# Kernel optimization log

Measured on AMD Instinct MI355X. Metric: run time of the kernel, lower is better.

The kernel has to match this reference:

```python
import jax, jax.numpy as jnp
import numpy as np

MARGIN = 0.3


def setup_inputs() -> dict:
    key = jax.random.key(0)
    k1, k2 = jax.random.split(key)
    inputs = jax.random.normal(k1, (8192, 256), dtype=jnp.float32)
    targets = jax.random.randint(k2, (8192,), 0, 512, dtype=jnp.int64)
    return {"inputs": inputs, "targets": targets}


def reference(inputs, targets):
    # L2-normalize features (normalize_feature=True default)
    x = inputs / (jnp.linalg.norm(inputs, axis=-1, keepdims=True) + 1e-12)
    n = x.shape[0]
    # pairwise euclidean distance [n, n]
    sq = jnp.sum(x * x, axis=1)
    dist = sq[:, None] + sq[None, :] - 2.0 * (x @ x.T)
    dist = jnp.sqrt(jnp.clip(dist, 1e-12, None))
    # positive / negative masks
    same = targets[:, None] == targets[None, :]
    eye = jnp.eye(n, dtype=bool)
    is_same = same & ~eye          # positives, diagonal excluded
    is_diff = ~same                # negatives
    neg_inf = jnp.float32(-jnp.inf)
    pos_inf = jnp.float32(jnp.inf)
    # hard positive: max over positives per row (fallback 0.0 if none)
    dist_ap = jnp.max(jnp.where(is_same, dist, neg_inf), axis=1)
    dist_ap = jnp.where(jnp.any(is_same, axis=1), dist_ap, 0.0)
    # hard negative: min over negatives per row (fallback margin+1 if none)
    dist_an = jnp.min(jnp.where(is_diff, dist, pos_inf), axis=1)
    dist_an = jnp.where(jnp.any(is_diff, axis=1), dist_an, MARGIN + 1.0)
    # MarginRankingLoss with y=1: mean(max(0, -(an - ap) + margin))
    loss = jnp.mean(jnp.maximum(0.0, dist_ap - dist_an + MARGIN))
    return loss
```

## Files before the change

### kernel.cpp

```cpp
#include <hip/hip_runtime.h>
#include <hip/hip_bf16.h>

#define NROWS  8192
#define DIM    256
#define MARGIN 0.3f

using bf16x8 = __attribute__((ext_vector_type(8))) short;
using f32x4  = __attribute__((ext_vector_type(4))) float;

__device__ inline ushort f2bf(float f) {
    __hip_bfloat16 h = __float2bfloat16(f);
    return *reinterpret_cast<ushort*>(&h);
}
__device__ inline float bf2f(ushort u) {
    return __uint_as_float(((unsigned)u) << 16);
}
__device__ inline unsigned f2ord(float f) {
    unsigned b = __float_as_uint(f);
    return (b & 0x80000000u) ? ~b : (b | 0x80000000u);
}
__device__ inline float ord2f(unsigned u) {
    return __uint_as_float((u & 0x80000000u) ? (u & 0x7FFFFFFFu) : ~u);
}
__device__ inline void ld16_g2l(const void* g, void* l) {
    __builtin_amdgcn_global_load_lds(
        (const __attribute__((address_space(1))) unsigned int*)g,
        (__attribute__((address_space(3))) unsigned int*)l, 16, 0, 0);
}

#define XBS_OFF 0u
#define SQS_OFF 4194304u
#define PMX_OFF 4259840u
#define NMN_OFF 4292608u
#define ACC_OFF 4327424u
#define TIK_OFF 4327432u

__global__ __launch_bounds__(256) void norm_kernel(
    const float* __restrict__ in, ushort* __restrict__ xbs,
    float* __restrict__ sqs, unsigned* __restrict__ pmax,
    unsigned* __restrict__ nmin, double* __restrict__ accd,
    unsigned* __restrict__ ticket)
{
    int row  = blockIdx.x * 4 + (threadIdx.x >> 6);
    int lane = threadIdx.x & 63;
    if (blockIdx.x == 0 && threadIdx.x == 0) { *accd = 0.0; *ticket = 0u; }
    float4 v = ((const float4*)(in + (size_t)row * DIM))[lane];
    float ss = v.x * v.x + v.y * v.y + v.z * v.z + v.w * v.w;
#pragma unroll
    for (int m = 1; m < 64; m <<= 1) ss += __shfl_xor(ss, m, 64);
    float inv = 1.0f / (sqrtf(ss) + 1e-12f);

    ushort4 st;
    st.x = f2bf(v.x * inv); st.y = f2bf(v.y * inv);
    st.z = f2bf(v.z * inv); st.w = f2bf(v.w * inv);

    ((ushort4*)(xbs + (size_t)row * DIM))[lane] = st;

    float a0 = bf2f(st.x), a1 = bf2f(st.y), a2 = bf2f(st.z), a3 = bf2f(st.w);
    float s2 = a0 * a0 + a1 * a1 + a2 * a2 + a3 * a3;
#pragma unroll
    for (int m = 1; m < 64; m <<= 1) s2 += __shfl_xor(s2, m, 64);
    if (lane == 0) {
        sqs[row]  = s2;
        pmax[row] = 0x007FFFFFu;
        nmin[row] = 0xFF800000u;
    }
}

__global__ __launch_bounds__(256, 2) void gram_kernel(
    const ushort* __restrict__ xbs, const float* __restrict__ sqs,
    const int* __restrict__ tgt, unsigned* __restrict__ pmax,
    unsigned* __restrict__ nmin)
{
    __shared__ struct {
        char  buf[2][16384];
        float sqc[512];
        int   tgc[512];
        int   tga[256];
    } sm;

    const int wave = threadIdx.x >> 6;
    const int lane = threadIdx.x & 63;
    const int l15  = lane & 15;
    const int quad = lane >> 4;
    const int mbase = blockIdx.x * 256 + wave * 64;
    const int nbase = blockIdx.y * 512;

    {
        int c = threadIdx.x * 2;
        sm.sqc[c]     = sqs[nbase + c];
        sm.sqc[c + 1] = sqs[nbase + c + 1];
        sm.tgc[c]     = tgt[nbase + c];
        sm.tgc[c + 1] = tgt[nbase + c + 1];
        sm.tga[threadIdx.x] = tgt[blockIdx.x * 256 + threadIdx.x];
    }

    bf16x8 afrag[4][8];
#pragma unroll
    for (int a = 0; a < 4; ++a) {
        const ushort* arow = xbs + (size_t)(mbase + a * 16 + l15) * DIM + quad * 8;
#pragma unroll
        for (int kk = 0; kk < 8; ++kk)
            afrag[a][kk] = *(const bf16x8*)(arow + kk * 32);
    }

    const int colh = lane >> 5, c31 = lane & 31;
    int offs[4];
#pragma unroll
    for (int j = 0; j < 4; ++j)
        offs[j] = colh * 512 + ((c31 ^ ((2 * j + colh) & 7)) << 4);

    const char* xbs_b = (const char*)xbs;

    {
        const char* gbase = xbs_b + (size_t)nbase * 512;
#pragma unroll
        for (int j = 0; j < 4; ++j) {
            int i = wave * 4 + j;
            ld16_g2l(gbase + i * 1024 + offs[j], sm.buf[0] + i * 1024);
        }
    }
    __syncthreads();

    float pm[16], nm[16];
#pragma unroll
    for (int j = 0; j < 16; ++j) { pm[j] = -__builtin_inff(); nm[j] = __builtin_inff(); }

#pragma unroll 2
    for (int s = 0; s < 16; ++s) {
        if (s < 15) {
            const char* gbase = xbs_b + (size_t)(nbase + (s + 1) * 32) * 512;
            char* lbase = sm.buf[(s + 1) & 1];
#pragma unroll
            for (int j = 0; j < 4; ++j) {
                int i = wave * 4 + j;
                ld16_g2l(gbase + i * 1024 + offs[j], lbase + i * 1024);
            }
        }
        const char* bufc = sm.buf[s & 1];
#pragma unroll
        for (int u = 0; u < 2; ++u) {
            const int t16 = s * 32 + u * 16;
            bf16x8 bfrag[8];
#pragma unroll
            for (int kk = 0; kk < 8; ++kk)
                bfrag[kk] = *(const bf16x8*)(bufc + u * 8192 + l15 * 512 +
                                             (((quad + 4 * kk) ^ (l15 & 7)) << 4));
            f32x4 acc4[4];
#pragma unroll
            for (int a = 0; a < 4; ++a) {
                f32x4 acc = {0.f, 0.f, 0.f, 0.f};
#pragma unroll
                for (int kk = 0; kk < 8; ++kk)
                    acc = __builtin_amdgcn_mfma_f32_16x16x32_bf16(afrag[a][kk], bfrag[kk], acc, 0, 0, 0);
                acc4[a] = acc;
            }
            const float sqc = sm.sqc[t16 + l15];
            const int   tc  = sm.tgc[t16 + l15];
#pragma unroll
            for (int a = 0; a < 4; ++a)
#pragma unroll
                for (int i = 0; i < 4; ++i) {
                    const float v = fmaf(acc4[a][i], -2.0f, sqc);
                    const bool same = (sm.tga[wave * 64 + a * 16 + quad * 4 + i] == tc);
                    pm[a * 4 + i] = fmaxf(pm[a * 4 + i], same ? v : -__builtin_inff());
                    nm[a * 4 + i] = fminf(nm[a * 4 + i], same ? __builtin_inff() : v);
                }
        }
        __syncthreads();
    }

#pragma unroll
    for (int m = 1; m < 16; m <<= 1) {
#pragma unroll
        for (int j = 0; j < 16; ++j) {
            pm[j] = fmaxf(pm[j], __shfl_xor(pm[j], m, 64));
            nm[j] = fminf(nm[j], __shfl_xor(nm[j], m, 64));
        }
    }
    if (l15 == 0) {
#pragma unroll
        for (int a = 0; a < 4; ++a)
#pragma unroll
            for (int i = 0; i < 4; ++i) {
                int r = mbase + a * 16 + quad * 4 + i;
                atomicMax(&pmax[r], f2ord(pm[a * 4 + i]));
                atomicMin(&nmin[r], f2ord(nm[a * 4 + i]));
            }
    }
}

__global__ __launch_bounds__(256) void finalize_kernel(
    const unsigned* __restrict__ pmax, const unsigned* __restrict__ nmin,
    const float* __restrict__ sqs, double* __restrict__ accd,
    unsigned* __restrict__ ticket, float* __restrict__ out)
{
    int r = blockIdx.x * 256 + threadIdx.x;
    float pe = ord2f(pmax[r]);
    float ne = ord2f(nmin[r]);
    float ap = sqrtf(fmaxf(sqs[r] + pe, 0.0f));
    float an = (ne > 1e30f) ? (MARGIN + 1.0f) : sqrtf(fmaxf(sqs[r] + ne, 0.0f));
    float h  = fmaxf(ap - an + MARGIN, 0.0f);
    double s = (double)h;
#pragma unroll
    for (int m = 1; m < 64; m <<= 1) s += __shfl_xor(s, m, 64);
    __shared__ double sh[4];
    if ((threadIdx.x & 63) == 0) sh[threadIdx.x >> 6] = s;
    __syncthreads();
    if (threadIdx.x == 0) {
        double b = sh[0] + sh[1] + sh[2] + sh[3];
        atomicAdd(accd, b);
        __threadfence();
        unsigned old = atomicAdd(ticket, 1u);
        if (old == gridDim.x - 1) {
            double total = atomicAdd(accd, 0.0);
            out[0] = (float)(total / (double)NROWS);
        }
    }
}

extern "C" void kernel_launch(void* const* d_in, const int* in_sizes, int n_in,
                              void* d_out, int out_size, void* d_ws, size_t ws_size,
                              hipStream_t stream) {
    const float* in  = (const float*)d_in[0];
    const int*   tgt = (const int*)d_in[1];
    float*       out = (float*)d_out;

    char* ws = (char*)d_ws;
    ushort*   xbs    = (ushort*)(ws + XBS_OFF);
    float*    sqs    = (float*)(ws + SQS_OFF);
    unsigned* pmax   = (unsigned*)(ws + PMX_OFF);
    unsigned* nmin   = (unsigned*)(ws + NMN_OFF);
    double*   accd   = (double*)(ws + ACC_OFF);
    unsigned* ticket = (unsigned*)(ws + TIK_OFF);

    norm_kernel<<<NROWS / 4, 256, 0, stream>>>(in, xbs, sqs, pmax, nmin, accd, ticket);
    gram_kernel<<<dim3(32, 16), 256, 0, stream>>>(xbs, sqs, tgt, pmax, nmin);
    finalize_kernel<<<32, 256, 0, stream>>>(pmax, nmin, sqs, accd, ticket, out);
}
```

Baseline: 108.3 us.

## Triple-buffer B tiles in gram kernel with one barrier per stage

Replaces the double-buffered LDS pipeline with a three-buffer ring that prefetches two stages ahead using global-to-LDS loads. Each stage now has a single s_barrier preceded by an explicit vmcnt wait, replacing the trailing __syncthreads. The goal is to hide global load latency and cut barrier stalls. In exchange, LDS use grows by 16KB per block, which may lower occupancy, and the loop is no longer unrolled.

```diff
diff --git a/kernel.cpp b/kernel.cpp
--- a/kernel.cpp
+++ b/kernel.cpp
@@ -73,7 +73,7 @@
     unsigned* __restrict__ nmin)
 {
     __shared__ struct {
-        char  buf[2][16384];
+        char  buf[3][16384];
         float sqc[512];
         int   tgc[512];
         int   tga[256];
@@ -113,11 +113,13 @@
     const char* xbs_b = (const char*)xbs;
 
     {
-        const char* gbase = xbs_b + (size_t)nbase * 512;
+        const char* g0 = xbs_b + (size_t)nbase * 512;
+        const char* g1 = xbs_b + (size_t)(nbase + 32) * 512;
 #pragma unroll
         for (int j = 0; j < 4; ++j) {
             int i = wave * 4 + j;
-            ld16_g2l(gbase + i * 1024 + offs[j], sm.buf[0] + i * 1024);
+            ld16_g2l(g0 + i * 1024 + offs[j], sm.buf[0] + i * 1024);
+            ld16_g2l(g1 + i * 1024 + offs[j], sm.buf[1] + i * 1024);
         }
     }
     __syncthreads();
@@ -126,49 +128,66 @@
 #pragma unroll
     for (int j = 0; j < 16; ++j) { pm[j] = -__builtin_inff(); nm[j] = __builtin_inff(); }
 
-#pragma unroll 2
-    for (int s = 0; s < 16; ++s) {
-        if (s < 15) {
-            const char* gbase = xbs_b + (size_t)(nbase + (s + 1) * 32) * 512;
-            char* lbase = sm.buf[(s + 1) & 1];
+#define COMPUTE_STAGE(bufc_, s_) do {                                        \
+        _Pragma("unroll")                                                    \
+        for (int u = 0; u < 2; ++u) {                                        \
+            const int t16 = (s_) * 32 + u * 16;                              \
+            bf16x8 bfrag[8];                                                 \
+            _Pragma("unroll")                                                \
+            for (int kk = 0; kk < 8; ++kk)                                   \
+                bfrag[kk] = *(const bf16x8*)((bufc_) + u * 8192 + l15 * 512 + \
+                                             (((quad + 4 * kk) ^ (l15 & 7)) << 4)); \
+            f32x4 acc4[4];                                                   \
+            _Pragma("unroll")                                                \
+            for (int a = 0; a < 4; ++a) {                                    \
+                f32x4 acc = {0.f, 0.f, 0.f, 0.f};                            \
+                _Pragma("unroll")                                            \
+                for (int kk = 0; kk < 8; ++kk)                               \
+                    acc = __builtin_amdgcn_mfma_f32_16x16x32_bf16(           \
+                              afrag[a][kk], bfrag[kk], acc, 0, 0, 0);        \
+                acc4[a] = acc;                                               \
+            }                                                                \
+            const float sqc = sm.sqc[t16 + l15];                             \
+            const int   tc  = sm.tgc[t16 + l15];                             \
+            _Pragma("unroll")                                                \
+            for (int a = 0; a < 4; ++a)                                      \
+                _Pragma("unroll")                                            \
+                for (int i = 0; i < 4; ++i) {                                \
+                    const float v = fmaf(acc4[a][i], -2.0f, sqc);            \
+                    const bool same = (sm.tga[wave * 64 + a * 16 + quad * 4 + i] == tc); \
+                    pm[a * 4 + i] = fmaxf(pm[a * 4 + i], same ? v : -__builtin_inff()); \
+                    nm[a * 4 + i] = fminf(nm[a * 4 + i], same ? __builtin_inff() : v);  \
+                }                                                            \
+        }                                                                    \
+    } while (0)
+
+    char* pA = sm.buf[0];
+    char* pB = sm.buf[1];
+    char* pC = sm.buf[2];
+
+#pragma unroll 1
+    for (int s = 0; s < 15; ++s) {
+        asm volatile("s_waitcnt vmcnt(4)" ::: "memory");
+        __builtin_amdgcn_sched_barrier(0);
+        __builtin_amdgcn_s_barrier();
+        __builtin_amdgcn_sched_barrier(0);
+        if (s < 14) {
+            const char* gbase = xbs_b + (size_t)(nbase + (s + 2) * 32) * 512;
 #pragma unroll
             for (int j = 0; j < 4; ++j) {
                 int i = wave * 4 + j;
-                ld16_g2l(gbase + i * 1024 + offs[j], lbase + i * 1024);
+                ld16_g2l(gbase + i * 1024 + offs[j], pC + i * 1024);
             }
         }
-        const char* bufc = sm.buf[s & 1];
-#pragma unroll
-        for (int u = 0; u < 2; ++u) {
-            const int t16 = s * 32 + u * 16;
-            bf16x8 bfrag[8];
-#pragma unroll
-            for (int kk = 0; kk < 8; ++kk)
-                bfrag[kk] = *(const bf16x8*)(bufc + u * 8192 + l15 * 512 +
-                                             (((quad + 4 * kk) ^ (l15 & 7)) << 4));
-            f32x4 acc4[4];
-#pragma unroll
-            for (int a = 0; a < 4; ++a) {
-                f32x4 acc = {0.f, 0.f, 0.f, 0.f};
-#pragma unroll
-                for (int kk = 0; kk < 8; ++kk)
-                    acc = __builtin_amdgcn_mfma_f32_16x16x32_bf16(afrag[a][kk], bfrag[kk], acc, 0, 0, 0);
-                acc4[a] = acc;
-            }
-            const float sqc = sm.sqc[t16 + l15];
-            const int   tc  = sm.tgc[t16 + l15];
-#pragma unroll
-            for (int a = 0; a < 4; ++a)
-#pragma unroll
-                for (int i = 0; i < 4; ++i) {
-                    const float v = fmaf(acc4[a][i], -2.0f, sqc);
-                    const bool same = (sm.tga[wave * 64 + a * 16 + quad * 4 + i] == tc);
-                    pm[a * 4 + i] = fmaxf(pm[a * 4 + i], same ? v : -__builtin_inff());
-                    nm[a * 4 + i] = fminf(nm[a * 4 + i], same ? __builtin_inff() : v);
-                }
-        }
-        __syncthreads();
-    }
+        COMPUTE_STAGE(pA, s);
+        char* t = pA; pA = pB; pB = pC; pC = t;
+    }
+    asm volatile("s_waitcnt vmcnt(0)" ::: "memory");
+    __builtin_amdgcn_sched_barrier(0);
+    __builtin_amdgcn_s_barrier();
+    __builtin_amdgcn_sched_barrier(0);
+    COMPUTE_STAGE(pA, 15);
+#undef COMPUTE_STAGE
 
 #pragma unroll
     for (int m = 1; m < 16; m <<= 1) {
```

Result: no change. 108.9 us (+0.5%).

## Exploit distance matrix symmetry by computing only lower-triangular tiles

Applied to the files above, without the earlier changes.

The Gram kernel now launches one block per lower-triangular 256x256 tile pair instead of the full matrix. Each tile updates both the row extrema and column extrema, the latter through shared-memory atomics and then global atomics. Full squared distances, including the row norm, are folded in so finalize no longer adds sqs. This roughly halves the MFMA work, at the cost of extra per-tile shuffles and atomics and a triangular index decode.

```diff
diff --git a/kernel.cpp b/kernel.cpp
--- a/kernel.cpp
+++ b/kernel.cpp
@@ -74,25 +74,34 @@
 {
     __shared__ struct {
         char  buf[2][16384];
-        float sqc[512];
-        int   tgc[512];
+        float sqc[256];
+        int   tgc[256];
         int   tga[256];
+        unsigned colp[256];
+        unsigned coln[256];
     } sm;
 
     const int wave = threadIdx.x >> 6;
     const int lane = threadIdx.x & 63;
     const int l15  = lane & 15;
     const int quad = lane >> 4;
-    const int mbase = blockIdx.x * 256 + wave * 64;
-    const int nbase = blockIdx.y * 512;
+
+    const int id = blockIdx.x;
+    int rb = (int)((sqrtf(8.0f * (float)id + 1.0f) - 1.0f) * 0.5f);
+    while ((rb + 1) * (rb + 2) / 2 <= id) ++rb;
+    while (rb * (rb + 1) / 2 > id) --rb;
+    const int cb = id - rb * (rb + 1) / 2;
+
+    const int mbase = rb * 256 + wave * 64;
+    const int nbase = cb * 256;
 
     {
-        int c = threadIdx.x * 2;
-        sm.sqc[c]     = sqs[nbase + c];
-        sm.sqc[c + 1] = sqs[nbase + c + 1];
-        sm.tgc[c]     = tgt[nbase + c];
-        sm.tgc[c + 1] = tgt[nbase + c + 1];
-        sm.tga[threadIdx.x] = tgt[blockIdx.x * 256 + threadIdx.x];
+        int c = threadIdx.x;
+        sm.sqc[c]  = sqs[nbase + c];
+        sm.tgc[c]  = tgt[nbase + c];
+        sm.tga[c]  = tgt[rb * 256 + c];
+        sm.colp[c] = 0x007FFFFFu;
+        sm.coln[c] = 0xFF800000u;
     }
 
     bf16x8 afrag[4][8];
@@ -103,6 +112,10 @@
         for (int kk = 0; kk < 8; ++kk)
             afrag[a][kk] = *(const bf16x8*)(arow + kk * 32);
     }
+    f32x4 sqa4[4];
+#pragma unroll
+    for (int a = 0; a < 4; ++a)
+        sqa4[a] = *(const f32x4*)(sqs + mbase + a * 16 + quad * 4);
 
     const int colh = lane >> 5, c31 = lane & 31;
     int offs[4];
@@ -127,8 +140,8 @@
     for (int j = 0; j < 16; ++j) { pm[j] = -__builtin_inff(); nm[j] = __builtin_inff(); }
 
 #pragma unroll 2
-    for (int s = 0; s < 16; ++s) {
-        if (s < 15) {
+    for (int s = 0; s < 8; ++s) {
+        if (s < 7) {
             const char* gbase = xbs_b + (size_t)(nbase + (s + 1) * 32) * 512;
             char* lbase = sm.buf[(s + 1) & 1];
 #pragma unroll
@@ -157,15 +170,28 @@
             }
             const float sqc = sm.sqc[t16 + l15];
             const int   tc  = sm.tgc[t16 + l15];
+            float cp = -__builtin_inff(), cn = __builtin_inff();
 #pragma unroll
             for (int a = 0; a < 4; ++a)
 #pragma unroll
                 for (int i = 0; i < 4; ++i) {
-                    const float v = fmaf(acc4[a][i], -2.0f, sqc);
+                    const float w = fmaf(acc4[a][i], -2.0f, sqa4[a][i] + sqc);
                     const bool same = (sm.tga[wave * 64 + a * 16 + quad * 4 + i] == tc);
-                    pm[a * 4 + i] = fmaxf(pm[a * 4 + i], same ? v : -__builtin_inff());
-                    nm[a * 4 + i] = fminf(nm[a * 4 + i], same ? __builtin_inff() : v);
+                    const float wp = same ? w : -__builtin_inff();
+                    const float wn = same ? __builtin_inff() : w;
+                    pm[a * 4 + i] = fmaxf(pm[a * 4 + i], wp);
+                    nm[a * 4 + i] = fminf(nm[a * 4 + i], wn);
+                    cp = fmaxf(cp, wp);
+                    cn = fminf(cn, wn);
                 }
+            cp = fmaxf(cp, __shfl_xor(cp, 16, 64));
+            cp = fmaxf(cp, __shfl_xor(cp, 32, 64));
+            cn = fminf(cn, __shfl_xor(cn, 16, 64));
+            cn = fminf(cn, __shfl_xor(cn, 32, 64));
+            if (quad == 0) {
+                atomicMax(&sm.colp[t16 + l15], f2ord(cp));
+                atomicMin(&sm.coln[t16 + l15], f2ord(cn));
+            }
         }
         __syncthreads();
     }
@@ -188,18 +214,20 @@
                 atomicMin(&nmin[r], f2ord(nm[a * 4 + i]));
             }
     }
+    atomicMax(&pmax[nbase + threadIdx.x], sm.colp[threadIdx.x]);
+    atomicMin(&nmin[nbase + threadIdx.x], sm.coln[threadIdx.x]);
 }
 
 __global__ __launch_bounds__(256) void finalize_kernel(
     const unsigned* __restrict__ pmax, const unsigned* __restrict__ nmin,
-    const float* __restrict__ sqs, double* __restrict__ accd,
-    unsigned* __restrict__ ticket, float* __restrict__ out)
+    double* __restrict__ accd, unsigned* __restrict__ ticket,
+    float* __restrict__ out)
 {
     int r = blockIdx.x * 256 + threadIdx.x;
     float pe = ord2f(pmax[r]);
     float ne = ord2f(nmin[r]);
-    float ap = sqrtf(fmaxf(sqs[r] + pe, 0.0f));
-    float an = (ne > 1e30f) ? (MARGIN + 1.0f) : sqrtf(fmaxf(sqs[r] + ne, 0.0f));
+    float ap = sqrtf(fmaxf(pe, 0.0f));
+    float an = (ne > 1e30f) ? (MARGIN + 1.0f) : sqrtf(fmaxf(ne, 0.0f));
     float h  = fmaxf(ap - an + MARGIN, 0.0f);
     double s = (double)h;
 #pragma unroll
@@ -235,6 +263,6 @@
     unsigned* ticket = (unsigned*)(ws + TIK_OFF);
 
     norm_kernel<<<NROWS / 4, 256, 0, stream>>>(in, xbs, sqs, pmax, nmin, accd, ticket);
-    gram_kernel<<<dim3(32, 16), 256, 0, stream>>>(xbs, sqs, tgt, pmax, nmin);
-    finalize_kernel<<<32, 256, 0, stream>>>(pmax, nmin, sqs, accd, ticket, out);
-}
+    gram_kernel<<<528, 256, 0, stream>>>(xbs, sqs, tgt, pmax, nmin);
+    finalize_kernel<<<32, 256, 0, stream>>>(pmax, nmin, accd, ticket, out);
+}
```

After: 246.5 us. 2.28x slower.
